# Kernel tuning notes

Hardware: AMD Instinct MI355X
Metric: run time of the kernel (lower is better)

## Reference

```python
import jax, jax.numpy as jnp
import numpy as np

L2_LAMDA = 0.001
RECONS_LAMDA = 0.2
LB_TH = 0.01
B, N, D = 32, 2048, 256


def setup_inputs() -> dict:
    key = jax.random.key(0)
    k1, k2, k3, k4 = jax.random.split(key, 4)
    cur = jax.random.normal(k1, (B, N, D), jnp.float32)
    pre = jax.random.normal(k2, (B, N, D), jnp.float32)
    lim_r = float(np.sqrt(6.0 / (D + D)))  # xavier_uniform bound
    r_proj = jax.random.uniform(k3, (D, D), jnp.float32, -lim_r, lim_r)
    lim_i = float(np.sqrt(6.0 / (N + N)))
    incidence_m = jax.random.uniform(k4, (N, N), jnp.float32, -lim_i, lim_i)
    return {"cur": cur, "pre": pre, "r_proj": r_proj, "incidence_m": incidence_m}


def reference(cur, pre, r_proj, incidence_m):
    # torch forward detaches cur/pre
    cur = jax.lax.stop_gradient(cur)
    pre = jax.lax.stop_gradient(pre)
    # clamp(min=lb_th) then zero where not (> lb_th)  ==  keep original where > lb_th else 0
    W = jnp.where(incidence_m > LB_TH, incidence_m, 0.0)          # (N, N)
    proj = jnp.einsum('bnd,de->bne', cur, r_proj)                 # (B, N, D)
    neigh = jnp.einsum('nm,bmd->bnd', W, pre)                     # (B, N, D)
    recon_err = jnp.sqrt(jnp.sum((proj - neigh) ** 2, axis=-1))   # (B, N)
    # torch: max(sum(abs(row[None,:]), dim=0)) == max-abs of the masked row
    l1 = jnp.max(jnp.abs(W), axis=1)                              # (N,)
    l2 = jnp.sqrt(jnp.sum(W ** 2, axis=1))                        # (N,)
    per_node = recon_err * RECONS_LAMDA + l1[None, :] + L2_LAMDA * l2[None, :]
    loss = jnp.sum(per_node, axis=1, keepdims=True)               # (B, 1)
    return loss, incidence_m
```

## Files before the change

kernel.cpp:

```cpp
#include <hip/hip_runtime.h>


typedef __attribute__((ext_vector_type(8))) short bf16x8;
typedef __attribute__((ext_vector_type(8))) unsigned short ushort8;
typedef __attribute__((ext_vector_type(4))) float f32x4;

__device__ __forceinline__ unsigned short f2bf(float f) {
    union { float f; unsigned u; } x; x.f = f;
    unsigned r = x.u + 0x7fffu + ((x.u >> 16) & 1u);
    return (unsigned short)(r >> 16);
}

#define GLL16(g, l)                                                         \
    __builtin_amdgcn_global_load_lds(                                       \
        (const __attribute__((address_space(1))) void*)(g),                 \
        (__attribute__((address_space(3))) void*)(l), 16, 0, 0)

__device__ __forceinline__ void transpose_64x64(
    const float* __restrict__ src, unsigned short* __restrict__ dst,
    int R, int C, int r0, int c0, unsigned short* __restrict__ tile) {
    const int t = threadIdx.x;
    const int fr = t >> 4, fc = (t & 15) * 4;
#pragma unroll
    for (int it = 0; it < 4; ++it) {
        int m = fr + it * 16;
        float4 v = *(const float4*)(src + (size_t)(r0 + m) * C + c0 + fc);
        unsigned short* p = tile + m * 66 + fc;
        ushort2 a, b;
        a.x = f2bf(v.x); a.y = f2bf(v.y);
        b.x = f2bf(v.z); b.y = f2bf(v.w);
        *(ushort2*)(p) = a;
        *(ushort2*)(p + 2) = b;
    }
    __syncthreads();
#pragma unroll
    for (int pss = 0; pss < 2; ++pss) {
        int d = (t >> 3) + pss * 32;
        int m8 = (t & 7) * 8;
        unsigned short r[8];
#pragma unroll
        for (int j = 0; j < 8; ++j) r[j] = tile[(m8 + j) * 66 + d];
        ushort8 pk;
        pk[0] = r[0]; pk[1] = r[1]; pk[2] = r[2]; pk[3] = r[3];
        pk[4] = r[4]; pk[5] = r[5]; pk[6] = r[6]; pk[7] = r[7];
        *(ushort8*)(dst + (size_t)(c0 + d) * R + r0 + m8) = pk;
    }
}

__global__ __launch_bounds__(256) void prep_all(
    const float* __restrict__ inc, float* __restrict__ out_inc,
    unsigned short* __restrict__ Wneg, float* __restrict__ crow,
    const float* __restrict__ cur, unsigned short* __restrict__ curb,
    const float* __restrict__ pre, unsigned short* __restrict__ preT,
    const float* __restrict__ r_proj, unsigned short* __restrict__ rprojT) {
    __shared__ unsigned short tile[64 * 66];
    __shared__ float smax[4], ssum[4];
    const int bid = blockIdx.x;
    const int t = threadIdx.x;

    if (bid < 2048) {
        const int row = bid;
        const float4* src = (const float4*)(inc + (size_t)row * 2048);
        float4* dst = (float4*)(out_inc + (size_t)row * 2048);
        ushort4* wp = (ushort4*)(Wneg + (size_t)row * 2048);
        float lmax = 0.f, ss = 0.f;
#pragma unroll
        for (int it = 0; it < 2; ++it) {
            int i = it * 256 + t;
            float4 v = src[i];
            dst[i] = v;
            float w0 = v.x > 0.01f ? v.x : 0.f;
            float w1 = v.y > 0.01f ? v.y : 0.f;
            float w2 = v.z > 0.01f ? v.z : 0.f;
            float w3 = v.w > 0.01f ? v.w : 0.f;
            ushort4 p;
            p.x = f2bf(-w0); p.y = f2bf(-w1); p.z = f2bf(-w2); p.w = f2bf(-w3);
            wp[i] = p;
            lmax = fmaxf(lmax, fmaxf(fmaxf(w0, w1), fmaxf(w2, w3)));
            ss += w0 * w0 + w1 * w1 + w2 * w2 + w3 * w3;
        }
#pragma unroll
        for (int off = 32; off; off >>= 1) {
            lmax = fmaxf(lmax, __shfl_down(lmax, off));
            ss += __shfl_down(ss, off);
        }
        int wv = t >> 6, ln = t & 63;
        if (ln == 0) { smax[wv] = lmax; ssum[wv] = ss; }
        __syncthreads();
        if (t == 0) {
            float m = fmaxf(fmaxf(smax[0], smax[1]), fmaxf(smax[2], smax[3]));
            float s = ssum[0] + ssum[1] + ssum[2] + ssum[3];
            crow[row] = m + 0.001f * sqrtf(s);
        }
    } else if (bid < 4096) {
        const size_t base = (size_t)(bid - 2048) * 2048;
#pragma unroll
        for (int it = 0; it < 8; ++it) {
            size_t i = base + it * 256 + t;
            float4 v = ((const float4*)cur)[i];
            ushort4 p;
            p.x = f2bf(v.x); p.y = f2bf(v.y); p.z = f2bf(v.z); p.w = f2bf(v.w);
            ((ushort4*)curb)[i] = p;
        }
    } else if (bid < 8192) {
        const int tt = bid - 4096;
        const int b = tt >> 7;
        const int mt = (tt & 127) >> 2;
        const int dt = tt & 3;
        transpose_64x64(pre + (size_t)b * 524288, preT + (size_t)b * 524288,
                        2048, 256, mt * 64, dt * 64, tile);
    } else {
        const int tt = bid - 8192;
        transpose_64x64(r_proj, rprojT, 256, 256, (tt >> 2) * 64, (tt & 3) * 64,
                        tile);
    }
}

__global__ __launch_bounds__(256, 2) void gemm_diff(
    const unsigned short* __restrict__ Wneg,
    const unsigned short* __restrict__ curb,
    const unsigned short* __restrict__ preT,
    const unsigned short* __restrict__ rprojT,
    float* __restrict__ Ssq)
{
    const int n0 = blockIdx.x * 128;
    const int b  = blockIdx.y;

    __shared__ unsigned short Al[128 * 32];
    __shared__ unsigned short Bl[256 * 32];
    __shared__ float ssq[128];

    const int tid  = threadIdx.x;
    const int w    = tid >> 6;
    const int lane = tid & 63;
    const int l16  = lane & 15;
    const int quad = lane >> 4;
    const int wm   = w >> 1, wn = w & 1;

    if (tid < 128) ssq[tid] = 0.f;

    f32x4 acc[4][8] = {};

    const unsigned short* curB = curb + (size_t)b * 2048 * 256;
    const unsigned short* preB = preT + (size_t)b * 256 * 2048;

    const int srow  = lane >> 2;
    const int sbyte = (lane & 3) * 16;

    for (int kt = 0; kt < 72; ++kt) {
        const unsigned short *ab, *bb;
        size_t as, bs;
        if (kt < 64) {
            const int k0 = kt * 32;
            ab = Wneg + (size_t)n0 * 2048 + k0; as = 2048;
            bb = preB + k0;                     bs = 2048;
        } else {
            const int kk = kt * 32 - 2048;
            ab = curB + (size_t)n0 * 256 + kk;  as = 256;
            bb = rprojT + kk;                   bs = 256;
        }
        __syncthreads();
#pragma unroll
        for (int j = 0; j < 2; ++j) {
            const int row = w * 32 + j * 16 + srow;
            GLL16((const char*)(ab + row * as) + sbyte,
                  (char*)Al + w * 2048 + j * 1024);
        }
#pragma unroll
        for (int j = 0; j < 4; ++j) {
            const int row = w * 64 + j * 16 + srow;
            GLL16((const char*)(bb + row * bs) + sbyte,
                  (char*)Bl + w * 4096 + j * 1024);
        }
        __syncthreads();

        bf16x8 af[4], bfr[8];
#pragma unroll
        for (int mi = 0; mi < 4; ++mi)
            af[mi] = *(const bf16x8*)(Al + (wm * 64 + mi * 16 + l16) * 32 + quad * 8);
#pragma unroll
        for (int ni = 0; ni < 8; ++ni)
            bfr[ni] = *(const bf16x8*)(Bl + (wn * 128 + ni * 16 + l16) * 32 + quad * 8);
#pragma unroll
        for (int mi = 0; mi < 4; ++mi)
#pragma unroll
            for (int ni = 0; ni < 8; ++ni)
                acc[mi][ni] = __builtin_amdgcn_mfma_f32_16x16x32_bf16(
                    af[mi], bfr[ni], acc[mi][ni], 0, 0, 0);
    }
    __syncthreads();

#pragma unroll
    for (int mi = 0; mi < 4; ++mi)
#pragma unroll
        for (int r = 0; r < 4; ++r) {
            float s = 0.f;
#pragma unroll
            for (int ni = 0; ni < 8; ++ni) {
                float v = acc[mi][ni][r];
                s += v * v;
            }
            s += __shfl_xor(s, 1);
            s += __shfl_xor(s, 2);
            s += __shfl_xor(s, 4);
            s += __shfl_xor(s, 8);
            if (l16 == 0)
                atomicAdd(&ssq[wm * 64 + mi * 16 + quad * 4 + r], s);
        }
    __syncthreads();
    if (tid < 128)
        Ssq[(size_t)b * 2048 + n0 + tid] = sqrtf(ssq[tid]);
}

__global__ void finalize(const float* __restrict__ Ssq,
                         const float* __restrict__ crow,
                         float* __restrict__ out) {
    const int b = blockIdx.x;
    float s1 = 0.f, s2 = 0.f;
    for (int i = threadIdx.x; i < 2048; i += 256) {
        s1 += Ssq[(size_t)b * 2048 + i];
        s2 += crow[i];
    }
#pragma unroll
    for (int off = 32; off; off >>= 1) {
        s1 += __shfl_down(s1, off);
        s2 += __shfl_down(s2, off);
    }
    __shared__ float sm1[4], sm2[4];
    int wv = threadIdx.x >> 6, ln = threadIdx.x & 63;
    if (ln == 0) { sm1[wv] = s1; sm2[wv] = s2; }
    __syncthreads();
    if (threadIdx.x == 0)
        out[b] = 0.2f * (sm1[0] + sm1[1] + sm1[2] + sm1[3])
               + (sm2[0] + sm2[1] + sm2[2] + sm2[3]);
}

extern "C" void kernel_launch(void* const* d_in, const int* in_sizes, int n_in,
                              void* d_out, int out_size, void* d_ws, size_t ws_size,
                              hipStream_t stream) {
    const float* cur    = (const float*)d_in[0];
    const float* pre    = (const float*)d_in[1];
    const float* r_proj = (const float*)d_in[2];
    const float* inc    = (const float*)d_in[3];
    float* out = (float*)d_out;

    char* ws = (char*)d_ws;
    unsigned short* Wneg   = (unsigned short*)(ws + 0);
    unsigned short* curb   = (unsigned short*)(ws + 8388608);
    unsigned short* preT   = (unsigned short*)(ws + 41943040);
    unsigned short* rprojT = (unsigned short*)(ws + 75497472);
    float*          Sbuf   = (float*)(ws + 75628544);
    float*          crow   = (float*)(ws + 75890688);

    prep_all<<<8208, 256, 0, stream>>>(inc, out + 32, Wneg, crow,
                                       cur, curb, pre, preT, r_proj, rprojT);
    gemm_diff<<<dim3(16, 32), 256, 0, stream>>>(Wneg, curb, preT, rprojT, Sbuf);
    finalize<<<32, 256, 0, stream>>>(Sbuf, crow, out);
}
```

Baseline: 255.4 us.

## Fuse cur bf16 conversion into GEMM, use 32x32x16 MFMA with K=64 tiles

```diff
diff --git a/kernel.cpp b/kernel.cpp
--- a/kernel.cpp
+++ b/kernel.cpp
@@ -3,7 +3,7 @@
 
 typedef __attribute__((ext_vector_type(8))) short bf16x8;
 typedef __attribute__((ext_vector_type(8))) unsigned short ushort8;
-typedef __attribute__((ext_vector_type(4))) float f32x4;
+typedef __attribute__((ext_vector_type(16))) float f32x16;
 
 __device__ __forceinline__ unsigned short f2bf(float f) {
     union { float f; unsigned u; } x; x.f = f;
@@ -25,35 +25,31 @@
     for (int it = 0; it < 4; ++it) {
         int m = fr + it * 16;
         float4 v = *(const float4*)(src + (size_t)(r0 + m) * C + c0 + fc);
-        unsigned short* p = tile + m * 66 + fc;
-        ushort2 a, b;
-        a.x = f2bf(v.x); a.y = f2bf(v.y);
-        b.x = f2bf(v.z); b.y = f2bf(v.w);
-        *(ushort2*)(p) = a;
-        *(ushort2*)(p + 2) = b;
-    }
-    __syncthreads();
-#pragma unroll
-    for (int pss = 0; pss < 2; ++pss) {
-        int d = (t >> 3) + pss * 32;
-        int m8 = (t & 7) * 8;
-        unsigned short r[8];
-#pragma unroll
-        for (int j = 0; j < 8; ++j) r[j] = tile[(m8 + j) * 66 + d];
-        ushort8 pk;
-        pk[0] = r[0]; pk[1] = r[1]; pk[2] = r[2]; pk[3] = r[3];
-        pk[4] = r[4]; pk[5] = r[5]; pk[6] = r[6]; pk[7] = r[7];
-        *(ushort8*)(dst + (size_t)(c0 + d) * R + r0 + m8) = pk;
-    }
+        tile[(fc + 0) * 68 + m] = f2bf(v.x);
+        tile[(fc + 1) * 68 + m] = f2bf(v.y);
+        tile[(fc + 2) * 68 + m] = f2bf(v.z);
+        tile[(fc + 3) * 68 + m] = f2bf(v.w);
+    }
+    __syncthreads();
+    const int d = t >> 2, m0 = (t & 3) * 16;
+    unsigned short v[16];
+#pragma unroll
+    for (int j = 0; j < 4; ++j)
+        *(ushort4*)(v + j * 4) = *(const ushort4*)(tile + d * 68 + m0 + j * 4);
+    unsigned short* dp = dst + (size_t)(c0 + d) * R + r0 + m0;
+    ushort8 p0, p1;
+#pragma unroll
+    for (int j = 0; j < 8; ++j) { p0[j] = v[j]; p1[j] = v[8 + j]; }
+    *(ushort8*)(dp) = p0;
+    *(ushort8*)(dp + 8) = p1;
 }
 
 __global__ __launch_bounds__(256) void prep_all(
     const float* __restrict__ inc, float* __restrict__ out_inc,
     unsigned short* __restrict__ Wneg, float* __restrict__ crow,
-    const float* __restrict__ cur, unsigned short* __restrict__ curb,
     const float* __restrict__ pre, unsigned short* __restrict__ preT,
     const float* __restrict__ r_proj, unsigned short* __restrict__ rprojT) {
-    __shared__ unsigned short tile[64 * 66];
+    __shared__ unsigned short tile[64 * 68];
     __shared__ float smax[4], ssum[4];
     const int bid = blockIdx.x;
     const int t = threadIdx.x;
@@ -92,25 +88,15 @@
             float s = ssum[0] + ssum[1] + ssum[2] + ssum[3];
             crow[row] = m + 0.001f * sqrtf(s);
         }
-    } else if (bid < 4096) {
-        const size_t base = (size_t)(bid - 2048) * 2048;
-#pragma unroll
-        for (int it = 0; it < 8; ++it) {
-            size_t i = base + it * 256 + t;
-            float4 v = ((const float4*)cur)[i];
-            ushort4 p;
-            p.x = f2bf(v.x); p.y = f2bf(v.y); p.z = f2bf(v.z); p.w = f2bf(v.w);
-            ((ushort4*)curb)[i] = p;
-        }
-    } else if (bid < 8192) {
-        const int tt = bid - 4096;
+    } else if (bid < 6144) {
+        const int tt = bid - 2048;
         const int b = tt >> 7;
         const int mt = (tt & 127) >> 2;
         const int dt = tt & 3;
         transpose_64x64(pre + (size_t)b * 524288, preT + (size_t)b * 524288,
                         2048, 256, mt * 64, dt * 64, tile);
     } else {
-        const int tt = bid - 8192;
+        const int tt = bid - 6144;
         transpose_64x64(r_proj, rprojT, 256, 256, (tt >> 2) * 64, (tt & 3) * 64,
                         tile);
     }
@@ -118,7 +104,7 @@
 
 __global__ __launch_bounds__(256, 2) void gemm_diff(
     const unsigned short* __restrict__ Wneg,
-    const unsigned short* __restrict__ curb,
+    const float* __restrict__ cur,
     const unsigned short* __restrict__ preT,
     const unsigned short* __restrict__ rprojT,
     float* __restrict__ Ssq)
@@ -126,86 +112,106 @@
     const int n0 = blockIdx.x * 128;
     const int b  = blockIdx.y;
 
-    __shared__ unsigned short Al[128 * 32];
-    __shared__ unsigned short Bl[256 * 32];
+    __shared__ unsigned short Al[128 * 64];
+    __shared__ unsigned short Bl[256 * 64];
     __shared__ float ssq[128];
 
     const int tid  = threadIdx.x;
     const int w    = tid >> 6;
     const int lane = tid & 63;
-    const int l16  = lane & 15;
-    const int quad = lane >> 4;
+    const int l32  = lane & 31;
+    const int half = lane >> 5;
     const int wm   = w >> 1, wn = w & 1;
 
     if (tid < 128) ssq[tid] = 0.f;
 
-    f32x4 acc[4][8] = {};
-
-    const unsigned short* curB = curb + (size_t)b * 2048 * 256;
+    f32x16 acc[2][4] = {};
+
+    const float*          curB = cur  + (size_t)b * 2048 * 256;
     const unsigned short* preB = preT + (size_t)b * 256 * 2048;
 
-    const int srow  = lane >> 2;
-    const int sbyte = (lane & 3) * 16;
-
-    for (int kt = 0; kt < 72; ++kt) {
-        const unsigned short *ab, *bb;
-        size_t as, bs;
-        if (kt < 64) {
-            const int k0 = kt * 32;
-            ab = Wneg + (size_t)n0 * 2048 + k0; as = 2048;
-            bb = preB + k0;                     bs = 2048;
+    const int grow  = lane >> 3;
+    const int gbyte = (lane & 7) * 16;
+
+    for (int kt = 0; kt < 36; ++kt) {
+        __syncthreads();
+        if (kt < 32) {
+            const int k0 = kt * 64;
+            const unsigned short* ab = Wneg + (size_t)n0 * 2048 + k0;
+#pragma unroll
+            for (int j = 0; j < 4; ++j) {
+                const int row = w * 32 + j * 8 + grow;
+                GLL16((const char*)(ab + (size_t)row * 2048) + gbyte,
+                      (char*)Al + w * 4096 + j * 1024);
+            }
+            const unsigned short* bb = preB + k0;
+#pragma unroll
+            for (int j = 0; j < 8; ++j) {
+                const int row = w * 64 + j * 8 + grow;
+                GLL16((const char*)(bb + (size_t)row * 2048) + gbyte,
+                      (char*)Bl + w * 8192 + j * 1024);
+            }
         } else {
-            const int kk = kt * 32 - 2048;
-            ab = curB + (size_t)n0 * 256 + kk;  as = 256;
-            bb = rprojT + kk;                   bs = 256;
+            const int kk = kt * 64 - 2048;
+            const int r16 = tid >> 4, k4 = tid & 15;
+#pragma unroll
+            for (int i = 0; i < 8; ++i) {
+                const int row = r16 + i * 16;
+                float4 v = *(const float4*)(curB + (size_t)(n0 + row) * 256 + kk + k4 * 4);
+                ushort4 p;
+                p.x = f2bf(v.x); p.y = f2bf(v.y); p.z = f2bf(v.z); p.w = f2bf(v.w);
+                *(ushort4*)(Al + row * 64 + k4 * 4) = p;
+            }
+            const unsigned short* bb = rprojT + kk;
+#pragma unroll
+            for (int j = 0; j < 8; ++j) {
+                const int row = w * 64 + j * 8 + grow;
+                GLL16((const char*)(bb + (size_t)row * 256) + gbyte,
+                      (char*)Bl + w * 8192 + j * 1024);
+            }
         }
         __syncthreads();
-#pragma unroll
-        for (int j = 0; j < 2; ++j) {
-            const int row = w * 32 + j * 16 + srow;
-            GLL16((const char*)(ab + row * as) + sbyte,
-                  (char*)Al + w * 2048 + j * 1024);
-        }
-#pragma unroll
-        for (int j = 0; j < 4; ++j) {
-            const int row = w * 64 + j * 16 + srow;
-            GLL16((const char*)(bb + row * bs) + sbyte,
-                  (char*)Bl + w * 4096 + j * 1024);
-        }
-        __syncthreads();
-
-        bf16x8 af[4], bfr[8];
-#pragma unroll
-        for (int mi = 0; mi < 4; ++mi)
-            af[mi] = *(const bf16x8*)(Al + (wm * 64 + mi * 16 + l16) * 32 + quad * 8);
-#pragma unroll
-        for (int ni = 0; ni < 8; ++ni)
-            bfr[ni] = *(const bf16x8*)(Bl + (wn * 128 + ni * 16 + l16) * 32 + quad * 8);
-#pragma unroll
-        for (int mi = 0; mi < 4; ++mi)
-#pragma unroll
-            for (int ni = 0; ni < 8; ++ni)
-                acc[mi][ni] = __builtin_amdgcn_mfma_f32_16x16x32_bf16(
-                    af[mi], bfr[ni], acc[mi][ni], 0, 0, 0);
-    }
-    __syncthreads();
-
-#pragma unroll
-    for (int mi = 0; mi < 4; ++mi)
-#pragma unroll
-        for (int r = 0; r < 4; ++r) {
+
+#pragma unroll
+        for (int ks = 0; ks < 4; ++ks) {
+            bf16x8 af[2], bfr[4];
+#pragma unroll
+            for (int mi = 0; mi < 2; ++mi)
+                af[mi] = *(const bf16x8*)(Al + (wm * 64 + mi * 32 + l32) * 64 +
+                                          ks * 16 + half * 8);
+#pragma unroll
+            for (int ni = 0; ni < 4; ++ni)
+                bfr[ni] = *(const bf16x8*)(Bl + (wn * 128 + ni * 32 + l32) * 64 +
+                                           ks * 16 + half * 8);
+#pragma unroll
+            for (int mi = 0; mi < 2; ++mi)
+#pragma unroll
+                for (int ni = 0; ni < 4; ++ni)
+                    acc[mi][ni] = __builtin_amdgcn_mfma_f32_32x32x16_bf16(
+                        af[mi], bfr[ni], acc[mi][ni], 0, 0, 0);
+        }
+    }
+    __syncthreads();
+
+#pragma unroll
+    for (int mi = 0; mi < 2; ++mi)
+#pragma unroll
+        for (int reg = 0; reg < 16; ++reg) {
             float s = 0.f;
 #pragma unroll
-            for (int ni = 0; ni < 8; ++ni) {
-                float v = acc[mi][ni][r];
+            for (int ni = 0; ni < 4; ++ni) {
+                float v = acc[mi][ni][reg];
                 s += v * v;
             }
             s += __shfl_xor(s, 1);
             s += __shfl_xor(s, 2);
             s += __shfl_xor(s, 4);
             s += __shfl_xor(s, 8);
-            if (l16 == 0)
-                atomicAdd(&ssq[wm * 64 + mi * 16 + quad * 4 + r], s);
+            s += __shfl_xor(s, 16);
+            if (l32 == 0) {
+                const int row = (reg & 3) + 8 * (reg >> 2) + 4 * half;
+                atomicAdd(&ssq[wm * 64 + mi * 32 + row], s);
+            }
         }
     __syncthreads();
     if (tid < 128)
@@ -246,14 +252,13 @@
 
     char* ws = (char*)d_ws;
     unsigned short* Wneg   = (unsigned short*)(ws + 0);
-    unsigned short* curb   = (unsigned short*)(ws + 8388608);
-    unsigned short* preT   = (unsigned short*)(ws + 41943040);
-    unsigned short* rprojT = (unsigned short*)(ws + 75497472);
-    float*          Sbuf   = (float*)(ws + 75628544);
-    float*          crow   = (float*)(ws + 75890688);
-
-    prep_all<<<8208, 256, 0, stream>>>(inc, out + 32, Wneg, crow,
-                                       cur, curb, pre, preT, r_proj, rprojT);
-    gemm_diff<<<dim3(16, 32), 256, 0, stream>>>(Wneg, curb, preT, rprojT, Sbuf);
+    unsigned short* preT   = (unsigned short*)(ws + 8388608);
+    unsigned short* rprojT = (unsigned short*)(ws + 41943040);
+    float*          Sbuf   = (float*)(ws + 42074112);
+    float*          crow   = (float*)(ws + 42336256);
+
+    prep_all<<<6160, 256, 0, stream>>>(inc, out + 32, Wneg, crow,
+                                       pre, preT, r_proj, rprojT);
+    gemm_diff<<<dim3(16, 32), 256, 0, stream>>>(Wneg, cur, preT, rprojT, Sbuf);
     finalize<<<32, 256, 0, stream>>>(Sbuf, crow, out);
 }
```

Result: slower. 284.1 us (+11.3%).

## Load A operand directly to registers and fuse cur bf16 conversion into GEMM

Applied to the files above, without the earlier changes.

```diff
diff --git a/kernel.cpp b/kernel.cpp
--- a/kernel.cpp
+++ b/kernel.cpp
@@ -25,35 +25,31 @@
     for (int it = 0; it < 4; ++it) {
         int m = fr + it * 16;
         float4 v = *(const float4*)(src + (size_t)(r0 + m) * C + c0 + fc);
-        unsigned short* p = tile + m * 66 + fc;
-        ushort2 a, b;
-        a.x = f2bf(v.x); a.y = f2bf(v.y);
-        b.x = f2bf(v.z); b.y = f2bf(v.w);
-        *(ushort2*)(p) = a;
-        *(ushort2*)(p + 2) = b;
-    }
-    __syncthreads();
-#pragma unroll
-    for (int pss = 0; pss < 2; ++pss) {
-        int d = (t >> 3) + pss * 32;
-        int m8 = (t & 7) * 8;
-        unsigned short r[8];
-#pragma unroll
-        for (int j = 0; j < 8; ++j) r[j] = tile[(m8 + j) * 66 + d];
-        ushort8 pk;
-        pk[0] = r[0]; pk[1] = r[1]; pk[2] = r[2]; pk[3] = r[3];
-        pk[4] = r[4]; pk[5] = r[5]; pk[6] = r[6]; pk[7] = r[7];
-        *(ushort8*)(dst + (size_t)(c0 + d) * R + r0 + m8) = pk;
-    }
+        tile[(fc + 0) * 68 + m] = f2bf(v.x);
+        tile[(fc + 1) * 68 + m] = f2bf(v.y);
+        tile[(fc + 2) * 68 + m] = f2bf(v.z);
+        tile[(fc + 3) * 68 + m] = f2bf(v.w);
+    }
+    __syncthreads();
+    const int d = t >> 2, m0 = (t & 3) * 16;
+    unsigned short v[16];
+#pragma unroll
+    for (int j = 0; j < 4; ++j)
+        *(ushort4*)(v + j * 4) = *(const ushort4*)(tile + d * 68 + m0 + j * 4);
+    unsigned short* dp = dst + (size_t)(c0 + d) * R + r0 + m0;
+    ushort8 p0, p1;
+#pragma unroll
+    for (int j = 0; j < 8; ++j) { p0[j] = v[j]; p1[j] = v[8 + j]; }
+    *(ushort8*)(dp) = p0;
+    *(ushort8*)(dp + 8) = p1;
 }
 
 __global__ __launch_bounds__(256) void prep_all(
     const float* __restrict__ inc, float* __restrict__ out_inc,
     unsigned short* __restrict__ Wneg, float* __restrict__ crow,
-    const float* __restrict__ cur, unsigned short* __restrict__ curb,
     const float* __restrict__ pre, unsigned short* __restrict__ preT,
     const float* __restrict__ r_proj, unsigned short* __restrict__ rprojT) {
-    __shared__ unsigned short tile[64 * 66];
+    __shared__ unsigned short tile[64 * 68];
     __shared__ float smax[4], ssum[4];
     const int bid = blockIdx.x;
     const int t = threadIdx.x;
@@ -92,25 +88,15 @@
             float s = ssum[0] + ssum[1] + ssum[2] + ssum[3];
             crow[row] = m + 0.001f * sqrtf(s);
         }
-    } else if (bid < 4096) {
-        const size_t base = (size_t)(bid - 2048) * 2048;
-#pragma unroll
-        for (int it = 0; it < 8; ++it) {
-            size_t i = base + it * 256 + t;
-            float4 v = ((const float4*)cur)[i];
-            ushort4 p;
-            p.x = f2bf(v.x); p.y = f2bf(v.y); p.z = f2bf(v.z); p.w = f2bf(v.w);
-            ((ushort4*)curb)[i] = p;
-        }
-    } else if (bid < 8192) {
-        const int tt = bid - 4096;
+    } else if (bid < 6144) {
+        const int tt = bid - 2048;
         const int b = tt >> 7;
         const int mt = (tt & 127) >> 2;
         const int dt = tt & 3;
         transpose_64x64(pre + (size_t)b * 524288, preT + (size_t)b * 524288,
                         2048, 256, mt * 64, dt * 64, tile);
     } else {
-        const int tt = bid - 8192;
+        const int tt = bid - 6144;
         transpose_64x64(r_proj, rprojT, 256, 256, (tt >> 2) * 64, (tt & 3) * 64,
                         tile);
     }
@@ -118,7 +104,7 @@
 
 __global__ __launch_bounds__(256, 2) void gemm_diff(
     const unsigned short* __restrict__ Wneg,
-    const unsigned short* __restrict__ curb,
+    const float* __restrict__ cur,
     const unsigned short* __restrict__ preT,
     const unsigned short* __restrict__ rprojT,
     float* __restrict__ Ssq)
@@ -126,7 +112,6 @@
     const int n0 = blockIdx.x * 128;
     const int b  = blockIdx.y;
 
-    __shared__ unsigned short Al[128 * 32];
     __shared__ unsigned short Bl[256 * 32];
     __shared__ float ssq[128];
 
@@ -141,43 +126,59 @@
 
     f32x4 acc[4][8] = {};
 
-    const unsigned short* curB = curb + (size_t)b * 2048 * 256;
+    const float*          curB = cur  + (size_t)b * 2048 * 256;
     const unsigned short* preB = preT + (size_t)b * 256 * 2048;
 
     const int srow  = lane >> 2;
     const int sbyte = (lane & 3) * 16;
 
+    const unsigned short* aW = Wneg + (size_t)(n0 + wm * 64 + l16) * 2048 + quad * 8;
+    const float*          aC = curB + (size_t)(n0 + wm * 64 + l16) * 256 + quad * 8;
+
     for (int kt = 0; kt < 72; ++kt) {
-        const unsigned short *ab, *bb;
-        size_t as, bs;
+        bf16x8 af[4];
         if (kt < 64) {
             const int k0 = kt * 32;
-            ab = Wneg + (size_t)n0 * 2048 + k0; as = 2048;
-            bb = preB + k0;                     bs = 2048;
+#pragma unroll
+            for (int mi = 0; mi < 4; ++mi)
+                af[mi] = *(const bf16x8*)(aW + (size_t)mi * 16 * 2048 + k0);
         } else {
             const int kk = kt * 32 - 2048;
-            ab = curB + (size_t)n0 * 256 + kk;  as = 256;
-            bb = rprojT + kk;                   bs = 256;
-        }
+#pragma unroll
+            for (int mi = 0; mi < 4; ++mi) {
+                const float* p = aC + (size_t)mi * 16 * 256 + kk;
+                float4 v0 = *(const float4*)(p);
+                float4 v1 = *(const float4*)(p + 4);
+                bf16x8 a;
+                a[0] = (short)f2bf(v0.x); a[1] = (short)f2bf(v0.y);
+                a[2] = (short)f2bf(v0.z); a[3] = (short)f2bf(v0.w);
+                a[4] = (short)f2bf(v1.x); a[5] = (short)f2bf(v1.y);
+                a[6] = (short)f2bf(v1.z); a[7] = (short)f2bf(v1.w);
+                af[mi] = a;
+            }
+        }
+
         __syncthreads();
-#pragma unroll
-        for (int j = 0; j < 2; ++j) {
-            const int row = w * 32 + j * 16 + srow;
-            GLL16((const char*)(ab + row * as) + sbyte,
-                  (char*)Al + w * 2048 + j * 1024);
-        }
-#pragma unroll
-        for (int j = 0; j < 4; ++j) {
-            const int row = w * 64 + j * 16 + srow;
-            GLL16((const char*)(bb + row * bs) + sbyte,
-                  (char*)Bl + w * 4096 + j * 1024);
+        if (kt < 64) {
+            const unsigned short* bb = preB + kt * 32;
+#pragma unroll
+            for (int j = 0; j < 4; ++j) {
+                const int row = w * 64 + j * 16 + srow;
+                GLL16((const char*)(bb + (size_t)row * 2048) + sbyte,
+                      (char*)Bl + w * 4096 + j * 1024);
+            }
+        } else {
+            const unsigned short* bb = rprojT + (kt * 32 - 2048);
+#pragma unroll
+            for (int j = 0; j < 4; ++j) {
+                const int row = w * 64 + j * 16 + srow;
+                GLL16((const char*)(bb + (size_t)row * 256) + sbyte,
+                      (char*)Bl + w * 4096 + j * 1024);
+            }
         }
         __syncthreads();
 
-        bf16x8 af[4], bfr[8];
-#pragma unroll
-        for (int mi = 0; mi < 4; ++mi)
-            af[mi] = *(const bf16x8*)(Al + (wm * 64 + mi * 16 + l16) * 32 + quad * 8);
+        bf16x8 bfr[8];
 #pragma unroll
         for (int ni = 0; ni < 8; ++ni)
             bfr[ni] = *(const bf16x8*)(Bl + (wn * 128 + ni * 16 + l16) * 32 + quad * 8);
@@ -246,14 +247,13 @@
 
     char* ws = (char*)d_ws;
     unsigned short* Wneg   = (unsigned short*)(ws + 0);
-    unsigned short* curb   = (unsigned short*)(ws + 8388608);
-    unsigned short* preT   = (unsigned short*)(ws + 41943040);
-    unsigned short* rprojT = (unsigned short*)(ws + 75497472);
-    float*          Sbuf   = (float*)(ws + 75628544);
-    float*          crow   = (float*)(ws + 75890688);
-
-    prep_all<<<8208, 256, 0, stream>>>(inc, out + 32, Wneg, crow,
-                                       cur, curb, pre, preT, r_proj, rprojT);
-    gemm_diff<<<dim3(16, 32), 256, 0, stream>>>(Wneg, curb, preT, rprojT, Sbuf);
+    unsigned short* preT   = (unsigned short*)(ws + 8388608);
+    unsigned short* rprojT = (unsigned short*)(ws + 41943040);
+    float*          Sbuf   = (float*)(ws + 42074112);
+    float*          crow   = (float*)(ws + 42336256);
+
+    prep_all<<<6160, 256, 0, stream>>>(inc, out + 32, Wneg, crow,
+                                       pre, preT, r_proj, rprojT);
+    gemm_diff<<<dim3(16, 32), 256, 0, stream>>>(Wneg, cur, preT, rprojT, Sbuf);
     finalize<<<32, 256, 0, stream>>>(Sbuf, crow, out);
 }
```

New measurement: 272.6 us. +6.7%, slower.
